# Kernel optimization log

Measured on AMD Instinct MI355X. Metric: run time of the kernel, lower is better.

The kernel has to match this reference:

```python
import jax, jax.numpy as jnp
import numpy as np

# irreps_in = 256x0e + 256x1o + 128x2e + 64x3o -> list of (mul, ir_dim=2l+1)
IRREPS = [(256, 1), (256, 3), (128, 5), (64, 7)]
DIM = sum(m * d for m, d in IRREPS)  # 2112
BATCH = 65536


def setup_inputs() -> dict:
    key = jax.random.key(0)
    features = jax.random.normal(key, (BATCH, DIM), dtype=jnp.float32)
    return {"features": features}


def reference(features):
    # Per-irrep squared-norm reduction then sqrt (equivalent to e3nn Norm).
    # For each (mul, d) block: [B, mul*d] -> [B, mul, d] -> sqrt(sum_d x^2)
    B = features.shape[0]
    outs = []
    off = 0
    for mul, d in IRREPS:
        blk = features[:, off:off + mul * d].reshape(B, mul, d)
        outs.append(jnp.sqrt(jnp.sum(blk * blk, axis=-1)))
        off += mul * d
    return jnp.concatenate(outs, axis=-1)  # [B, sum(mul)] = [B, 704]
```

## Files before the change

### kernel.cpp

```cpp
#include <hip/hip_runtime.h>
#include <math.h>

#define ROW_DIM 2112
#define OUT_DIM 704
#define BLOCK 256

__global__ __launch_bounds__(BLOCK) void slownorm_kernel(
    const float* __restrict__ in, float* __restrict__ out)
{
    __shared__ float row[ROW_DIM];

    const int b = blockIdx.x;
    const float* __restrict__ src = in + (size_t)b * ROW_DIM;

    const float4* __restrict__ src4 = (const float4*)src;
    float4* row4 = (float4*)row;
    #pragma unroll
    for (int i = threadIdx.x; i < ROW_DIM / 4; i += BLOCK) {
        row4[i] = src4[i];
    }
    __syncthreads();

    float* __restrict__ dst = out + (size_t)b * OUT_DIM;

    for (int o = threadIdx.x; o < OUT_DIM; o += BLOCK) {
        int off, d, idx;
        if (o < 256)      { d = 1; off = 0;    idx = o;       }
        else if (o < 512) { d = 3; off = 256;  idx = o - 256; }
        else if (o < 640) { d = 5; off = 1024; idx = o - 512; }
        else              { d = 7; off = 1664; idx = o - 640; }

        const float* p = row + off + idx * d;
        float s = 0.0f;
        #pragma unroll 7
        for (int k = 0; k < d; ++k) s += p[k] * p[k];
        dst[o] = sqrtf(s);
    }
}

extern "C" void kernel_launch(void* const* d_in, const int* in_sizes, int n_in,
                              void* d_out, int out_size, void* d_ws, size_t ws_size,
                              hipStream_t stream)
{
    const float* features = (const float*)d_in[0];
    float* out = (float*)d_out;
    const int batch = in_sizes[0] / ROW_DIM;
    slownorm_kernel<<<batch, BLOCK, 0, stream>>>(features, out);
}
```

Before: 729.1 us.

## Replace per-row LDS staging with grid-stride float4 outputs grouped by irrep

Each thread now produces one float4 of output, four consecutive norms, and reads the input float4s it needs straight from global memory. This drops the shared-memory row staging and the block barrier. Work is laid out irrep-major across the whole batch in a persistent grid-stride loop capped at 2048 blocks, so each wavefront runs a single branch. In exchange, loads within a wavefront are strided by 3, 5 or 7 float4s for the higher irreps, which can lower coalescing efficiency. Each irrep group also reads rows in a separate pass, so cache reuse across the four passes of a row is lost.

After: 756.6 us. +3.8%, slower.

```diff
diff --git a/kernel.cpp b/kernel.cpp
--- a/kernel.cpp
+++ b/kernel.cpp
@@ -1,40 +1,71 @@
 #include <hip/hip_runtime.h>
 #include <math.h>
 
-#define ROW_DIM 2112
-#define OUT_DIM 704
+
+#define ROW4  528
+#define OUT4  176
 #define BLOCK 256
+#define GRID  2048
 
 __global__ __launch_bounds__(BLOCK) void slownorm_kernel(
-    const float* __restrict__ in, float* __restrict__ out)
+    const float4* __restrict__ in, float4* __restrict__ out, unsigned int batch)
 {
-    __shared__ float row[ROW_DIM];
+    const size_t n1 = (size_t)batch << 6;
+    const size_t n3 = (size_t)batch << 6;
+    const size_t n5 = (size_t)batch << 5;
+    const size_t n7 = (size_t)batch << 4;
+    const size_t b13  = n1 + n3;
+    const size_t b135 = b13 + n5;
+    const size_t ntot = b135 + n7;
 
-    const int b = blockIdx.x;
-    const float* __restrict__ src = in + (size_t)b * ROW_DIM;
+    const size_t stride = (size_t)gridDim.x * BLOCK;
+    for (size_t i = (size_t)blockIdx.x * BLOCK + threadIdx.x; i < ntot; i += stride) {
+        size_t row;
+        int    slot;
+        float4 r;
 
-    const float4* __restrict__ src4 = (const float4*)src;
-    float4* row4 = (float4*)row;
-    #pragma unroll
-    for (int i = threadIdx.x; i < ROW_DIM / 4; i += BLOCK) {
-        row4[i] = src4[i];
-    }
-    __syncthreads();
+        if (i < n1) {
+            row = i >> 6;
+            const int s = (int)(i & 63);
+            const float4 a = in[row * ROW4 + s];
+            r.x = fabsf(a.x); r.y = fabsf(a.y); r.z = fabsf(a.z); r.w = fabsf(a.w);
+            slot = s;
+        } else if (i < b13) {
+            const size_t j = i - n1;
+            row = j >> 6;
+            const int s = (int)(j & 63);
+            const float4* __restrict__ p = in + row * ROW4 + 64 + (size_t)s * 3;
+            const float4 a = p[0], b = p[1], c = p[2];
+            r.x = sqrtf(a.x*a.x + a.y*a.y + a.z*a.z);
+            r.y = sqrtf(a.w*a.w + b.x*b.x + b.y*b.y);
+            r.z = sqrtf(b.z*b.z + b.w*b.w + c.x*c.x);
+            r.w = sqrtf(c.y*c.y + c.z*c.z + c.w*c.w);
+            slot = 64 + s;
+        } else if (i < b135) {
+            const size_t j = i - b13;
+            row = j >> 5;
+            const int s = (int)(j & 31);
+            const float4* __restrict__ p = in + row * ROW4 + 256 + (size_t)s * 5;
+            const float4 a = p[0], b = p[1], c = p[2], d = p[3], e = p[4];
+            r.x = sqrtf(a.x*a.x + a.y*a.y + a.z*a.z + a.w*a.w + b.x*b.x);
+            r.y = sqrtf(b.y*b.y + b.z*b.z + b.w*b.w + c.x*c.x + c.y*c.y);
+            r.z = sqrtf(c.z*c.z + c.w*c.w + d.x*d.x + d.y*d.y + d.z*d.z);
+            r.w = sqrtf(d.w*d.w + e.x*e.x + e.y*e.y + e.z*e.z + e.w*e.w);
+            slot = 128 + s;
+        } else {
+            const size_t j = i - b135;
+            row = j >> 4;
+            const int s = (int)(j & 15);
+            const float4* __restrict__ p = in + row * ROW4 + 416 + (size_t)s * 7;
+            const float4 a = p[0], b = p[1], c = p[2], d = p[3], e = p[4], f = p[5], g = p[6];
+            r.x = sqrtf(a.x*a.x + a.y*a.y + a.z*a.z + a.w*a.w + b.x*b.x + b.y*b.y + b.z*b.z);
+            r.y = sqrtf(b.w*b.w + c.x*c.x + c.y*c.y + c.z*c.z + c.w*c.w + d.x*d.x + d.y*d.y);
+            r.z = sqrtf(d.z*d.z + d.w*d.w + e.x*e.x + e.y*e.y + e.z*e.z + e.w*e.w + f.x*f.x);
+            r.w = sqrtf(f.y*f.y + f.z*f.z + f.w*f.w + g.x*g.x + g.y*g.y + g.z*g.z + g.w*g.w);
+            slot = 160 + s;
+        }
 
-    float* __restrict__ dst = out + (size_t)b * OUT_DIM;
-
-    for (int o = threadIdx.x; o < OUT_DIM; o += BLOCK) {
-        int off, d, idx;
-        if (o < 256)      { d = 1; off = 0;    idx = o;       }
-        else if (o < 512) { d = 3; off = 256;  idx = o - 256; }
-        else if (o < 640) { d = 5; off = 1024; idx = o - 512; }
-        else              { d = 7; off = 1664; idx = o - 640; }
-
-        const float* p = row + off + idx * d;
-        float s = 0.0f;
-        #pragma unroll 7
-        for (int k = 0; k < d; ++k) s += p[k] * p[k];
-        dst[o] = sqrtf(s);
+        out[row * OUT4 + slot] = r;
     }
 }
 
@@ -42,8 +73,13 @@
                               void* d_out, int out_size, void* d_ws, size_t ws_size,
                               hipStream_t stream)
 {
-    const float* features = (const float*)d_in[0];
-    float* out = (float*)d_out;
-    const int batch = in_sizes[0] / ROW_DIM;
-    slownorm_kernel<<<batch, BLOCK, 0, stream>>>(features, out);
+    const float4* in  = (const float4*)d_in[0];
+    float4*       out = (float4*)d_out;
+    const unsigned int batch = (unsigned int)(in_sizes[0] / 2112);
+
+    const size_t ntot = (size_t)batch * 176;
+    unsigned int grid = (unsigned int)((ntot + BLOCK - 1) / BLOCK);
+    if (grid > GRID) grid = GRID;
+
+    slownorm_kernel<<<grid, BLOCK, 0, stream>>>(in, out, batch);
 }
```
